# Optimization experiments

Hardware: AMD Instinct MI355X
Metric: run time of the kernel (lower is better)

## Reference

```python
import jax, jax.numpy as jnp
import numpy as np

QMIN, QMAX = -128, 127  # int8 asymmetric range used by torchao per-token quant
EPS = float(np.finfo(np.float32).eps)


def per_token_dynamic_quant(x):
    # choose_qparams_per_token_asymmetric (torchao) followed by quantize+dequantize
    min_val = jnp.min(x, axis=-1, keepdims=True)
    max_val = jnp.max(x, axis=-1, keepdims=True)
    min_neg = jnp.minimum(min_val, 0.0)
    max_pos = jnp.maximum(max_val, 0.0)
    scale = (max_pos - min_neg) / float(QMAX - QMIN)
    scale = jnp.maximum(scale, EPS)
    desc_min = min_neg / scale
    desc_max = max_pos / scale
    zp = jnp.where((QMIN + desc_min) + (QMAX + desc_max) > 0,
                   QMIN - desc_min, QMAX - desc_max)
    zp = jnp.clip(jnp.round(zp), QMIN, QMAX)
    q = jnp.clip(jnp.round(x / scale) + zp, QMIN, QMAX)
    return (q - zp) * scale  # fake-quantized activations, same dtype as x


def setup_inputs() -> dict:
    key = jax.random.key(0)
    k1, k2, k3 = jax.random.split(key, 3)
    TOKENS, IN_F, OUT_F = 8192, 4096, 11008
    x = jax.random.normal(k1, (TOKENS, IN_F), dtype=jnp.float32)
    weight_int8 = jax.random.randint(k2, (OUT_F, IN_F), -128, 128, dtype=jnp.int32).astype(jnp.int8)
    scales = jax.random.uniform(k3, (OUT_F,), dtype=jnp.float32, minval=1e-3, maxval=2e-2)
    zeros = jnp.zeros((OUT_F,), dtype=jnp.float32)
    return {"x": x, "weight_int8": weight_int8, "scales": scales, "zeros": zeros}


def reference(x, weight_int8, scales, zeros):
    # per-token dynamic fake quant of activations
    x_dq = per_token_dynamic_quant(x.astype(jnp.float32))
    # per-channel (axis 0) weight dequant: (w - zero) * scale
    w_dq = (weight_int8.astype(jnp.float32) - zeros[:, None]) * scales[:, None]  # [out, in]
    # F.linear: x @ w.T
    return jnp.einsum('ti,oi->to', x_dq, w_dq)
```

## Files before the change

kernel.cpp:

```cpp
#include <hip/hip_runtime.h>

#define TOKENS 8192
#define KDIM   4096
#define OUTF   11008

typedef int int4v __attribute__((ext_vector_type(4)));

__global__ __launch_bounds__(256) void quant_x_kernel(
    const float* __restrict__ x, char* __restrict__ q8,
    float* __restrict__ sc, float* __restrict__ zpv, int* __restrict__ qsum)
{
    const int t = blockIdx.x;
    const int tid = threadIdx.x;
    const float4* xr = (const float4*)(x + (size_t)t * KDIM);

    float4 v[4];
    float mn = 3.0e38f, mx = -3.0e38f;
#pragma unroll
    for (int j = 0; j < 4; ++j) {
        v[j] = xr[tid + 256 * j];
        mn = fminf(mn, fminf(fminf(v[j].x, v[j].y), fminf(v[j].z, v[j].w)));
        mx = fmaxf(mx, fmaxf(fmaxf(v[j].x, v[j].y), fmaxf(v[j].z, v[j].w)));
    }
#pragma unroll
    for (int off = 32; off > 0; off >>= 1) {
        mn = fminf(mn, __shfl_down(mn, off, 64));
        mx = fmaxf(mx, __shfl_down(mx, off, 64));
    }
    __shared__ float smn[4], smx[4];
    __shared__ int ssum[4];
    if ((tid & 63) == 0) { smn[tid >> 6] = mn; smx[tid >> 6] = mx; }
    __syncthreads();
    mn = fminf(fminf(smn[0], smn[1]), fminf(smn[2], smn[3]));
    mx = fmaxf(fmaxf(smx[0], smx[1]), fmaxf(smx[2], smx[3]));

    const float min_neg = fminf(mn, 0.0f);
    const float max_pos = fmaxf(mx, 0.0f);
    float scale = (max_pos - min_neg) / 255.0f;
    scale = fmaxf(scale, 1.1920928955078125e-07f);
    const float dmin = min_neg / scale;
    const float dmax = max_pos / scale;
    float zpf = ((-128.0f + dmin) + (127.0f + dmax) > 0.0f) ? (-128.0f - dmin)
                                                            : (127.0f - dmax);
    zpf = fminf(fmaxf(rintf(zpf), -128.0f), 127.0f);
    const float inv = 1.0f / scale;

    int s = 0;
    int* qrow = (int*)(q8 + (size_t)t * KDIM);
#pragma unroll
    for (int j = 0; j < 4; ++j) {
        int q0 = (int)fminf(fmaxf(rintf(v[j].x * inv) + zpf, -128.0f), 127.0f);
        int q1 = (int)fminf(fmaxf(rintf(v[j].y * inv) + zpf, -128.0f), 127.0f);
        int q2 = (int)fminf(fmaxf(rintf(v[j].z * inv) + zpf, -128.0f), 127.0f);
        int q3 = (int)fminf(fmaxf(rintf(v[j].w * inv) + zpf, -128.0f), 127.0f);
        s += q0 + q1 + q2 + q3;
        qrow[tid + 256 * j] = (q0 & 255) | ((q1 & 255) << 8) | ((q2 & 255) << 16) | (q3 << 24);
    }
#pragma unroll
    for (int off = 32; off > 0; off >>= 1) s += __shfl_down(s, off, 64);
    if ((tid & 63) == 0) ssum[tid >> 6] = s;
    __syncthreads();
    if (tid == 0) {
        sc[t] = scale;
        zpv[t] = zpf;
        qsum[t] = ssum[0] + ssum[1] + ssum[2] + ssum[3];
    }
}

__global__ __launch_bounds__(256) void pack_w_kernel(
    const int* __restrict__ w, char* __restrict__ w8, int* __restrict__ wsum)
{
    const int o = blockIdx.x;
    const int tid = threadIdx.x;
    const int4* wr = (const int4*)(w + (size_t)o * KDIM);
    int* dst = (int*)(w8 + (size_t)o * KDIM);
    int s = 0;
#pragma unroll
    for (int j = 0; j < 4; ++j) {
        int4 a = wr[tid + 256 * j];
        s += a.x + a.y + a.z + a.w;
        dst[tid + 256 * j] = (a.x & 255) | ((a.y & 255) << 8) | ((a.z & 255) << 16) | (a.w << 24);
    }
#pragma unroll
    for (int off = 32; off > 0; off >>= 1) s += __shfl_down(s, off, 64);
    __shared__ int ss[4];
    if ((tid & 63) == 0) ss[tid >> 6] = s;
    __syncthreads();
    if (tid == 0) wsum[o] = ss[0] + ss[1] + ss[2] + ss[3];
}

__device__ __forceinline__ void async_cp16(const void* g, void* l) {
    __builtin_amdgcn_global_load_lds(
        (const __attribute__((address_space(1))) void*)g,
        (__attribute__((address_space(3))) void*)l, 16, 0, 0);
}

__global__ __launch_bounds__(256) void gemm_i8_kernel(
    const char* __restrict__ q8, const char* __restrict__ w8,
    const float* __restrict__ sc, const float* __restrict__ zpv,
    const int* __restrict__ qsum,
    const float* __restrict__ scales, const float* __restrict__ zeros,
    const int* __restrict__ wsum, float* __restrict__ out)
{
    const int tid = threadIdx.x;
    const int wave = tid >> 6;
    const int lane = tid & 63;
    const int o0 = blockIdx.x * 128;
    const int t0 = blockIdx.y * 128;

    __shared__ char smem[128 * 128 * 2];
    char* sA = smem;
    char* sB = smem + 128 * 128;

    const char* Ag = q8 + (size_t)t0 * KDIM;
    const char* Bg = w8 + (size_t)o0 * KDIM;

    const int wm = (wave & 1) * 64;
    const int wn = (wave >> 1) * 64;
    const int lr = lane & 15;
    const int kq = lane >> 4;
    const int swz = lr & 7;

    int4v acc[4][4];
#pragma unroll
    for (int mi = 0; mi < 4; ++mi)
#pragma unroll
        for (int ni = 0; ni < 4; ++ni)
            acc[mi][ni] = (int4v){0, 0, 0, 0};

    for (int k0 = 0; k0 < KDIM; k0 += 128) {
#pragma unroll
        for (int it = 0; it < 4; ++it) {
            const int idx = it * 256 + tid;
            const int r = idx >> 3;
            const int cs = ((idx & 7) ^ (r & 7)) << 4;
            async_cp16(Ag + (size_t)r * KDIM + k0 + cs, sA + idx * 16);
        }
#pragma unroll
        for (int it = 0; it < 4; ++it) {
            const int idx = it * 256 + tid;
            const int r = idx >> 3;
            const int cs = ((idx & 7) ^ (r & 7)) << 4;
            async_cp16(Bg + (size_t)r * KDIM + k0 + cs, sB + idx * 16);
        }
        __builtin_amdgcn_s_waitcnt(0);
        __syncthreads();

#pragma unroll
        for (int kk = 0; kk < 128; kk += 64) {
            const int coff = (((kk >> 4) + kq) ^ swz) << 4;
            int4v a[4], b[4];
#pragma unroll
            for (int mi = 0; mi < 4; ++mi)
                a[mi] = *(const int4v*)(sA + (wm + mi * 16 + lr) * 128 + coff);
#pragma unroll
            for (int ni = 0; ni < 4; ++ni)
                b[ni] = *(const int4v*)(sB + (wn + ni * 16 + lr) * 128 + coff);
#pragma unroll
            for (int mi = 0; mi < 4; ++mi)
#pragma unroll
                for (int ni = 0; ni < 4; ++ni)
                    acc[mi][ni] = __builtin_amdgcn_mfma_i32_16x16x64_i8(
                        a[mi], b[ni], acc[mi][ni], 0, 0, 0);
        }
        __syncthreads();
    }

#pragma unroll
    for (int mi = 0; mi < 4; ++mi) {
        const int tb = t0 + wm + mi * 16 + ((lane >> 4) << 2);
        float st4[4], zp4[4], qs4[4];
        int zi4[4];
#pragma unroll
        for (int r = 0; r < 4; ++r) {
            st4[r] = sc[tb + r];
            zp4[r] = zpv[tb + r];
            zi4[r] = (int)zp4[r];
            qs4[r] = (float)qsum[tb + r];
        }
#pragma unroll
        for (int ni = 0; ni < 4; ++ni) {
            const int o = o0 + wn + ni * 16 + lr;
            const float so = scales[o];
            const float zo = zeros[o];
            const long long wso = (long long)wsum[o];
#pragma unroll
            for (int r = 0; r < 4; ++r) {
                long long iv = (long long)acc[mi][ni][r] - (long long)zi4[r] * wso;
                float val = (float)iv - zo * (qs4[r] - 4096.0f * zp4[r]);
                out[(size_t)(tb + r) * OUTF + o] = st4[r] * so * val;
            }
        }
    }
}

extern "C" void kernel_launch(void* const* d_in, const int* in_sizes, int n_in,
                              void* d_out, int out_size, void* d_ws, size_t ws_size,
                              hipStream_t stream) {
    const float* x      = (const float*)d_in[0];
    const int*   w      = (const int*)d_in[1];
    const float* scales = (const float*)d_in[2];
    const float* zeros  = (const float*)d_in[3];
    float* out = (float*)d_out;

    char* ws = (char*)d_ws;
    char*  q8   = ws;
    char*  w8   = ws + 33554432;
    float* sc   = (float*)(ws + 78643200);
    float* zp   = (float*)(ws + 78675968);
    int*   qsum = (int*)(ws + 78708736);
    int*   wsum = (int*)(ws + 78741504);

    quant_x_kernel<<<TOKENS, 256, 0, stream>>>(x, q8, sc, zp, qsum);
    pack_w_kernel<<<OUTF, 256, 0, stream>>>(w, w8, wsum);
    dim3 grid(OUTF / 128, TOKENS / 128);
    gemm_i8_kernel<<<grid, 256, 0, stream>>>(q8, w8, sc, zp, qsum, scales, zeros, wsum, out);
}
```

Before: 1.089 ms.

## Pipeline int8 GEMM with 4-stage async LDS ring and 256x256 tiles

The int8 GEMM is restructured to use 256x256 output tiles per 512-thread block, with each wave computing a 128x64 sub-tile. K is split into 64-wide steps fed through a 4-deep ring of LDS buffers, using async global-to-LDS loads and partial vmcnt waits so loads overlap the MFMA work. A grouped block-index swizzle is added for L2 reuse, and s_setprio is raised around the MFMA bursts. The goal is to remove the previous load-wait-compute serialization and to raise arithmetic intensity per byte staged. The cost is 128KB of LDS per block, which limits occupancy, plus higher accumulator register pressure.

```diff
diff --git a/kernel.cpp b/kernel.cpp
--- a/kernel.cpp
+++ b/kernel.cpp
@@ -3,6 +3,7 @@
 #define TOKENS 8192
 #define KDIM   4096
 #define OUTF   11008
+#define NTILE  64
 
 typedef int int4v __attribute__((ext_vector_type(4)));
 
@@ -95,7 +96,48 @@
         (__attribute__((address_space(3))) void*)l, 16, 0, 0);
 }
 
-__global__ __launch_bounds__(256) void gemm_i8_kernel(
+#define STAGE(T)                                                                \
+    do {                                                                        \
+        char* dA_ = smem + ((T) & 3) * 32768;                                   \
+        char* dB_ = dA_ + 16384;                                                \
+        const int k0_ = (T) * 64;                                               \
+        _Pragma("unroll")                                                       \
+        for (int it_ = 0; it_ < 2; ++it_) {                                     \
+            const int idx_ = it_ * 512 + tid;                                   \
+            const int r_ = idx_ >> 2;                                           \
+            const int cs_ = (((idx_ & 3) ^ ((r_ >> 1) & 3)) << 4);              \
+            async_cp16(Ag + (size_t)r_ * KDIM + k0_ + cs_, dA_ + idx_ * 16);    \
+            async_cp16(Bg + (size_t)r_ * KDIM + k0_ + cs_, dB_ + idx_ * 16);    \
+        }                                                                       \
+    } while (0)
+
+#define COMPUTE(T)                                                              \
+    do {                                                                        \
+        const char* sA_ = smem + ((T) & 3) * 32768;                             \
+        const char* sB_ = sA_ + 16384;                                          \
+        int4v a_[8], b_[4];                                                     \
+        _Pragma("unroll")                                                       \
+        for (int mi_ = 0; mi_ < 8; ++mi_)                                       \
+            a_[mi_] = *(const int4v*)(sA_ + (wm + mi_ * 16 + lr) * 64 + coff);  \
+        _Pragma("unroll")                                                       \
+        for (int ni_ = 0; ni_ < 4; ++ni_)                                       \
+            b_[ni_] = *(const int4v*)(sB_ + (wn + ni_ * 16 + lr) * 64 + coff);  \
+        __builtin_amdgcn_s_setprio(1);                                          \
+        _Pragma("unroll")                                                       \
+        for (int mi_ = 0; mi_ < 8; ++mi_)                                       \
+            _Pragma("unroll")                                                   \
+            for (int ni_ = 0; ni_ < 4; ++ni_)                                   \
+                acc[mi_][ni_] = __builtin_amdgcn_mfma_i32_16x16x64_i8(          \
+                    a_[mi_], b_[ni_], acc[mi_][ni_], 0, 0, 0);                  \
+        __builtin_amdgcn_s_setprio(0);                                          \
+    } while (0)
+
+#define WAIT_BAR(N)                                                             \
+    asm volatile("s_waitcnt vmcnt(" #N ")" ::: "memory");                       \
+    __builtin_amdgcn_s_barrier();                                               \
+    __builtin_amdgcn_sched_barrier(0);
+
+__global__ __launch_bounds__(512, 2) void gemm_i8_kernel(
     const char* __restrict__ q8, const char* __restrict__ w8,
     const float* __restrict__ sc, const float* __restrict__ zpv,
     const int* __restrict__ qsum,
@@ -105,70 +147,49 @@
     const int tid = threadIdx.x;
     const int wave = tid >> 6;
     const int lane = tid & 63;
-    const int o0 = blockIdx.x * 128;
-    const int t0 = blockIdx.y * 128;
-
-    __shared__ char smem[128 * 128 * 2];
-    char* sA = smem;
-    char* sB = smem + 128 * 128;
+
+    const int bid = blockIdx.x;
+    const int swz = (bid & 7) * 172 + (bid >> 3);
+    const int by = swz / 43;
+    const int bx = swz - by * 43;
+    const int t0 = by * 256;
+    const int o0 = bx * 256;
+
+    __shared__ char smem[131072];
 
     const char* Ag = q8 + (size_t)t0 * KDIM;
     const char* Bg = w8 + (size_t)o0 * KDIM;
 
-    const int wm = (wave & 1) * 64;
-    const int wn = (wave >> 1) * 64;
+    const int wm = (wave >> 2) * 128;
+    const int wn = (wave & 3) * 64;
     const int lr = lane & 15;
     const int kq = lane >> 4;
-    const int swz = lr & 7;
-
-    int4v acc[4][4];
-#pragma unroll
-    for (int mi = 0; mi < 4; ++mi)
+    const int coff = ((kq ^ ((lr >> 1) & 3)) << 4);
+
+    int4v acc[8][4];
+#pragma unroll
+    for (int mi = 0; mi < 8; ++mi)
 #pragma unroll
         for (int ni = 0; ni < 4; ++ni)
             acc[mi][ni] = (int4v){0, 0, 0, 0};
 
-    for (int k0 = 0; k0 < KDIM; k0 += 128) {
-#pragma unroll
-        for (int it = 0; it < 4; ++it) {
-            const int idx = it * 256 + tid;
-            const int r = idx >> 3;
-            const int cs = ((idx & 7) ^ (r & 7)) << 4;
-            async_cp16(Ag + (size_t)r * KDIM + k0 + cs, sA + idx * 16);
-        }
-#pragma unroll
-        for (int it = 0; it < 4; ++it) {
-            const int idx = it * 256 + tid;
-            const int r = idx >> 3;
-            const int cs = ((idx & 7) ^ (r & 7)) << 4;
-            async_cp16(Bg + (size_t)r * KDIM + k0 + cs, sB + idx * 16);
-        }
-        __builtin_amdgcn_s_waitcnt(0);
-        __syncthreads();
-
-#pragma unroll
-        for (int kk = 0; kk < 128; kk += 64) {
-            const int coff = (((kk >> 4) + kq) ^ swz) << 4;
-            int4v a[4], b[4];
-#pragma unroll
-            for (int mi = 0; mi < 4; ++mi)
-                a[mi] = *(const int4v*)(sA + (wm + mi * 16 + lr) * 128 + coff);
-#pragma unroll
-            for (int ni = 0; ni < 4; ++ni)
-                b[ni] = *(const int4v*)(sB + (wn + ni * 16 + lr) * 128 + coff);
-#pragma unroll
-            for (int mi = 0; mi < 4; ++mi)
-#pragma unroll
-                for (int ni = 0; ni < 4; ++ni)
-                    acc[mi][ni] = __builtin_amdgcn_mfma_i32_16x16x64_i8(
-                        a[mi], b[ni], acc[mi][ni], 0, 0, 0);
-        }
-        __syncthreads();
-    }
-
-#pragma unroll
-    for (int mi = 0; mi < 4; ++mi) {
-        const int tb = t0 + wm + mi * 16 + ((lane >> 4) << 2);
+    STAGE(0); STAGE(1); STAGE(2);
+
+    for (int t = 0; t < NTILE - 3; ++t) {
+        WAIT_BAR(8)
+        STAGE(t + 3);
+        COMPUTE(t);
+    }
+    WAIT_BAR(8)
+    COMPUTE(NTILE - 3);
+    WAIT_BAR(4)
+    COMPUTE(NTILE - 2);
+    WAIT_BAR(0)
+    COMPUTE(NTILE - 1);
+
+#pragma unroll
+    for (int mi = 0; mi < 8; ++mi) {
+        const int tb = t0 + wm + mi * 16 + (kq << 2);
         float st4[4], zp4[4], qs4[4];
         int zi4[4];
 #pragma unroll
@@ -213,6 +234,5 @@
 
     quant_x_kernel<<<TOKENS, 256, 0, stream>>>(x, q8, sc, zp, qsum);
     pack_w_kernel<<<OUTF, 256, 0, stream>>>(w, w8, wsum);
-    dim3 grid(OUTF / 128, TOKENS / 128);
-    gemm_i8_kernel<<<grid, 256, 0, stream>>>(q8, w8, sc, zp, qsum, scales, zeros, wsum, out);
-}
+    gemm_i8_kernel<<<dim3(1376), 512, 0, stream>>>(q8, w8, sc, zp, qsum, scales, zeros, wsum, out);
+}
```

New measurement: 909.3 us. 16.5% less time.
